# Performance work log

Hardware: AMD Instinct MI355X
Metric: run time of the kernel (lower is better)

The kernel has to match this reference:

```python
import jax, jax.numpy as jnp
import numpy as np

N_ATOMS = 524288
D = 256
B = 16384  # number of molecules (segments)
M_STEPS = 6


def setup_inputs() -> dict:
    key = jax.random.key(0)
    k1, k2, k3 = jax.random.split(key, 3)
    atom_features = jax.random.normal(k1, (N_ATOMS, D), dtype=jnp.float32)
    atom_split = jnp.sort(jax.random.randint(k2, (N_ATOMS,), 0, B, dtype=jnp.int32))
    # LSTM weights: U is (2d, 4d); bias has forget gate initialized to 1
    U = jax.random.normal(k3, (2 * D, 4 * D), dtype=jnp.float32) * (1.0 / np.sqrt(2 * D))
    b = jnp.concatenate([
        jnp.zeros((D,), jnp.float32),
        jnp.ones((D,), jnp.float32),
        jnp.zeros((D,), jnp.float32),
        jnp.zeros((D,), jnp.float32),
    ])
    return {"atom_features": atom_features, "atom_split": atom_split, "U": U, "b": b}


def _lstm_step(q_star, c, U, b):
    z = q_star @ U + b  # [B, 4d]
    i = jax.nn.sigmoid(z[:, :D])
    f = jax.nn.sigmoid(z[:, D:2 * D])
    o = jax.nn.sigmoid(z[:, 2 * D:3 * D])
    g = jnp.tanh(z[:, 3 * D:])
    c_out = f * c + i * g
    h_out = o * jnp.tanh(c_out)
    return h_out, c_out


def reference(atom_features, atom_split, U, b):
    c = jnp.zeros((B, D), jnp.float32)
    h = jnp.zeros((B, D), jnp.float32)
    q_star = None
    for _ in range(M_STEPS):
        q_expanded = h[atom_split]                     # [N, d] gather
        e = jnp.sum(atom_features * q_expanded, axis=1)  # [N]
        e_exp = jnp.exp(e)
        e_mol = jax.ops.segment_sum(e_exp, atom_split, num_segments=B)  # [B]
        a = e_exp / e_mol[atom_split]                  # segment softmax [N]
        r = jax.ops.segment_sum(a[:, None] * atom_features, atom_split, num_segments=B)  # [B, d]
        q_star = jnp.concatenate([h, r], axis=1)       # [B, 2d]
        h, c = _lstm_step(q_star, c, U, b)
    return q_star
```

## Files before the change

### kernel.cpp

```cpp
#include <hip/hip_runtime.h>
#include <hip/hip_bf16.h>
#include <math.h>

#define N_ATOMS 524288
#define DIM 256
#define NB 16384
#define M_STEPS 6

typedef _Float16 f16x8 __attribute__((ext_vector_type(8)));
typedef float f32x16 __attribute__((ext_vector_type(16)));

__device__ __forceinline__ float sigmoidf_(float z) {
    return 1.0f / (1.0f + __expf(-z));
}
__device__ __forceinline__ float tanh_fast(float z) {
    return 1.0f - 2.0f / (__expf(2.0f * z) + 1.0f);
}
__device__ __forceinline__ float2 h2f2(unsigned u) {
    union { unsigned u; _Float16 h[2]; } x; x.u = u;
    float2 r; r.x = (float)x.h[0]; r.y = (float)x.h[1]; return r;
}

__global__ void bounds_kernel(const int* __restrict__ split, int* __restrict__ lb) {
    int b = blockIdx.x * blockDim.x + threadIdx.x;
    if (b > NB) return;
    int lo = 0, hi = N_ATOMS;
    while (lo < hi) {
        int mid = (lo + hi) >> 1;
        if (split[mid] < b) lo = mid + 1; else hi = mid;
    }
    lb[b] = lo;
}

__global__ __launch_bounds__(256) void uswz_kernel(const float* __restrict__ U,
                                                   _Float16* __restrict__ uh) {
    int d = blockIdx.x * 256 + threadIdx.x;
    int f = d >> 8;
    int r = d & 255;
    int jjp = r >> 6;
    int lane = r & 63;
    int nt = f >> 5, kc = f & 31;
    int n = nt * 32 + (lane & 31);
    int k = kc * 16 + (lane >> 5) * 8 + jjp * 2;
    union { unsigned u; _Float16 h[2]; } p;
    p.h[0] = (_Float16)U[(size_t)k * 1024 + n];
    p.h[1] = (_Float16)U[(size_t)(k + 1) * 1024 + n];
    *(unsigned*)(&uh[(size_t)(f * 64 + lane) * 8 + jjp * 2]) = p.u;
}

__global__ __launch_bounds__(256) void attn0_cvt_kernel(
    const float* __restrict__ x,
    const int* __restrict__ lb,
    float* __restrict__ rout,
    _Float16* __restrict__ xh)
{
    const int t    = threadIdx.x;
    const int wave = t >> 6;
    const int lane = t & 63;
    const int b    = blockIdx.x * 4 + wave;
    const int g    = lane >> 4;
    const int q    = lane & 15;

    const int s = lb[b];
    const int e = lb[b + 1];

    float a0x=0.f,a0y=0.f,a0z=0.f,a0w=0.f;
    float a1x=0.f,a1y=0.f,a1z=0.f,a1w=0.f;
    float a2x=0.f,a2y=0.f,a2z=0.f,a2w=0.f;
    float a3x=0.f,a3y=0.f,a3z=0.f,a3w=0.f;
    float cnt = 0.f;

    for (int i = s + g; i < e; i += 4) {
        const float* xr = &x[(size_t)i * DIM + q * 16];
        const float4 c0 = *(const float4*)(xr + 0);
        const float4 c1 = *(const float4*)(xr + 4);
        const float4 c2 = *(const float4*)(xr + 8);
        const float4 c3 = *(const float4*)(xr + 12);
        cnt += 1.f;
        a0x += c0.x; a0y += c0.y; a0z += c0.z; a0w += c0.w;
        a1x += c1.x; a1y += c1.y; a1z += c1.z; a1w += c1.w;
        a2x += c2.x; a2y += c2.y; a2z += c2.z; a2w += c2.w;
        a3x += c3.x; a3y += c3.y; a3z += c3.z; a3w += c3.w;
        union { _Float16 h[16]; uint4 v[2]; } P;
        P.h[0]=(_Float16)c0.x; P.h[1]=(_Float16)c0.y; P.h[2]=(_Float16)c0.z; P.h[3]=(_Float16)c0.w;
        P.h[4]=(_Float16)c1.x; P.h[5]=(_Float16)c1.y; P.h[6]=(_Float16)c1.z; P.h[7]=(_Float16)c1.w;
        P.h[8]=(_Float16)c2.x; P.h[9]=(_Float16)c2.y; P.h[10]=(_Float16)c2.z; P.h[11]=(_Float16)c2.w;
        P.h[12]=(_Float16)c3.x; P.h[13]=(_Float16)c3.y; P.h[14]=(_Float16)c3.z; P.h[15]=(_Float16)c3.w;
        uint4* xw = (uint4*)(&xh[(size_t)i * DIM + q * 16]);
        xw[0] = P.v[0];
        xw[1] = P.v[1];
    }

#define XRED(v) { v += __shfl_xor(v, 16, 64); v += __shfl_xor(v, 32, 64); }
    XRED(a0x) XRED(a0y) XRED(a0z) XRED(a0w)
    XRED(a1x) XRED(a1y) XRED(a1z) XRED(a1w)
    XRED(a2x) XRED(a2y) XRED(a2z) XRED(a2w)
    XRED(a3x) XRED(a3y) XRED(a3z) XRED(a3w)
    XRED(cnt)
#undef XRED

    const float inv = (cnt > 0.f) ? (1.0f / cnt) : 0.f;
    float vx = (g==0) ? a0x : (g==1) ? a1x : (g==2) ? a2x : a3x;
    float vy = (g==0) ? a0y : (g==1) ? a1y : (g==2) ? a2y : a3y;
    float vz = (g==0) ? a0z : (g==1) ? a1z : (g==2) ? a2z : a3z;
    float vw = (g==0) ? a0w : (g==1) ? a1w : (g==2) ? a2w : a3w;
    float4 v; v.x = vx*inv; v.y = vy*inv; v.z = vz*inv; v.w = vw*inv;
    *(float4*)(&rout[(size_t)b * DIM + q * 16 + g * 4]) = v;
}

__global__ __launch_bounds__(256) void attn_f16_kernel(
    const _Float16* __restrict__ xhp,
    const int* __restrict__ lb,
    const float* __restrict__ h,
    float* __restrict__ rout,
    int rstride)
{
    const int t    = threadIdx.x;
    const int wave = t >> 6;
    const int lane = t & 63;
    const int b    = blockIdx.x * 4 + wave;
    const int g    = lane >> 4;
    const int q    = lane & 15;

    const int s = lb[b];
    const int e = lb[b + 1];

    const float* hrow = &h[(size_t)b * DIM + q * 16];
    const float4 hv0 = *(const float4*)(hrow + 0);
    const float4 hv1 = *(const float4*)(hrow + 4);
    const float4 hv2 = *(const float4*)(hrow + 8);
    const float4 hv3 = *(const float4*)(hrow + 12);

    float a0x=0.f,a0y=0.f,a0z=0.f,a0w=0.f;
    float a1x=0.f,a1y=0.f,a1z=0.f,a1w=0.f;
    float a2x=0.f,a2y=0.f,a2z=0.f,a2w=0.f;
    float a3x=0.f,a3y=0.f,a3z=0.f,a3w=0.f;
    float ssum = 0.f;

    int i = s + g;
    uint4 A = {0,0,0,0}, B = {0,0,0,0};
    if (i < e) {
        const uint4* xr = (const uint4*)(&xhp[(size_t)i * DIM + q * 16]);
        A = xr[0]; B = xr[1];
    }
    while (i < e) {
        const int inext = i + 4;
        const int iload = (inext < e) ? inext : i;
        const uint4* xr = (const uint4*)(&xhp[(size_t)iload * DIM + q * 16]);
        const uint4 nA = xr[0];
        const uint4 nB = xr[1];

        const float2 p0 = h2f2(A.x), p1 = h2f2(A.y), p2 = h2f2(A.z), p3 = h2f2(A.w);
        const float2 p4 = h2f2(B.x), p5 = h2f2(B.y), p6 = h2f2(B.z), p7 = h2f2(B.w);
        const float4 c0 = {p0.x, p0.y, p1.x, p1.y};
        const float4 c1 = {p2.x, p2.y, p3.x, p3.y};
        const float4 c2 = {p4.x, p4.y, p5.x, p5.y};
        const float4 c3 = {p6.x, p6.y, p7.x, p7.y};

        float d01 = c0.x*hv0.x + c0.y*hv0.y + c0.z*hv0.z + c0.w*hv0.w
                  + c1.x*hv1.x + c1.y*hv1.y + c1.z*hv1.z + c1.w*hv1.w;
        float d23 = c2.x*hv2.x + c2.y*hv2.y + c2.z*hv2.z + c2.w*hv2.w
                  + c3.x*hv3.x + c3.y*hv3.y + c3.z*hv3.z + c3.w*hv3.w;
        float d = d01 + d23;
        d += __shfl_xor(d, 1, 64);
        d += __shfl_xor(d, 2, 64);
        d += __shfl_xor(d, 4, 64);
        d += __shfl_xor(d, 8, 64);
        const float ee = __expf(d);
        ssum += ee;
        a0x += ee*c0.x; a0y += ee*c0.y; a0z += ee*c0.z; a0w += ee*c0.w;
        a1x += ee*c1.x; a1y += ee*c1.y; a1z += ee*c1.z; a1w += ee*c1.w;
        a2x += ee*c2.x; a2y += ee*c2.y; a2z += ee*c2.z; a2w += ee*c2.w;
        a3x += ee*c3.x; a3y += ee*c3.y; a3z += ee*c3.z; a3w += ee*c3.w;

        A = nA; B = nB;
        i = inext;
    }

#define XRED(v) { v += __shfl_xor(v, 16, 64); v += __shfl_xor(v, 32, 64); }
    XRED(a0x) XRED(a0y) XRED(a0z) XRED(a0w)
    XRED(a1x) XRED(a1y) XRED(a1z) XRED(a1w)
    XRED(a2x) XRED(a2y) XRED(a2z) XRED(a2w)
    XRED(a3x) XRED(a3y) XRED(a3z) XRED(a3w)
    XRED(ssum)
#undef XRED

    const float inv = (ssum > 0.f) ? (1.0f / ssum) : 0.f;
    float vx = (g==0) ? a0x : (g==1) ? a1x : (g==2) ? a2x : a3x;
    float vy = (g==0) ? a0y : (g==1) ? a1y : (g==2) ? a2y : a3y;
    float vz = (g==0) ? a0z : (g==1) ? a1z : (g==2) ? a2z : a3z;
    float vw = (g==0) ? a0w : (g==1) ? a1w : (g==2) ? a2w : a3w;
    float4 v; v.x = vx*inv; v.y = vy*inv; v.z = vz*inv; v.w = vw*inv;
    *(float4*)(&rout[(size_t)b * rstride + q * 16 + g * 4]) = v;
}

#define LBM 128
#define LBK 64
#define APAD 8
__global__ __launch_bounds__(256, 2) void lstm_mfma_kernel(
    const float* __restrict__ h_in,
    const float* __restrict__ r,
    const _Float16* __restrict__ uh,
    const float* __restrict__ bias,
    float* __restrict__ c,
    float* __restrict__ h_out,
    float* __restrict__ hdup,
    int kb0)
{
    __shared__ _Float16 As[LBM][LBK + APAD];
    __shared__ _Float16 Bs[8 * 4 * 512];

    const int t = threadIdx.x;
    const int w = t >> 6;
    const int lane = t & 63;
    const int m0 = blockIdx.y * LBM;
    const int bx = blockIdx.x;

    f32x16 acc[8];
    #pragma unroll
    for (int et = 0; et < 8; ++et)
        #pragma unroll
        for (int q = 0; q < 16; ++q) acc[et][q] = 0.0f;

    for (int kb = kb0; kb < 8; ++kb) {
        const float* A = (kb < 4) ? h_in : r;
        const int ak = (kb & 3) * LBK;
        __syncthreads();
        #pragma unroll
        for (int i = 0; i < 8; ++i) {
            int idx = i * 256 + t;
            int row = idx >> 4, k4 = idx & 15;
            float4 v = *(const float4*)(&A[(size_t)(m0 + row) * DIM + ak + k4 * 4]);
            union { _Float16 h[4]; ushort4 u; } bh;
            bh.h[0] = (_Float16)v.x; bh.h[1] = (_Float16)v.y;
            bh.h[2] = (_Float16)v.z; bh.h[3] = (_Float16)v.w;
            *(ushort4*)(&As[row][k4 * 4]) = bh.u;
        }
        #pragma unroll
        for (int run = 0; run < 8; ++run) {
            const int nt = (run >> 1) * 8 + bx * 2 + (run & 1);
            const uint4 v = ((const uint4*)(uh + (size_t)(nt * 32 + kb * 4) * 512))[t];
            *(uint4*)(&Bs[run * 2048 + t * 8]) = v;
        }
        __syncthreads();
        #pragma unroll
        for (int kc = 0; kc < 4; ++kc) {
            f16x8 af = *(const f16x8*)(&As[w * 32 + (lane & 31)][kc * 16 + (lane >> 5) * 8]);
            #pragma unroll
            for (int et = 0; et < 8; ++et) {
                f16x8 bh = *(const f16x8*)(&Bs[et * 2048 + kc * 512 + lane * 8]);
                acc[et] = __builtin_amdgcn_mfma_f32_32x32x16_f16(af, bh, acc[et], 0, 0, 0);
            }
        }
    }

    const int col32 = lane & 31;
    const int rbase = m0 + w * 32 + 4 * (lane >> 5);
    #pragma unroll
    for (int jh = 0; jh < 2; ++jh) {
        const int col = bx * 64 + jh * 32 + col32;
        const float bi = bias[col];
        const float bf_ = bias[256 + col];
        const float bo = bias[512 + col];
        const float bg = bias[768 + col];
        const f32x16 zi = acc[0 * 2 + jh];
        const f32x16 zf = acc[1 * 2 + jh];
        const f32x16 zo = acc[2 * 2 + jh];
        const f32x16 zg = acc[3 * 2 + jh];
        #pragma unroll
        for (int reg = 0; reg < 16; ++reg) {
            const int row = rbase + (reg & 3) + 8 * (reg >> 2);
            const size_t idx = (size_t)row * DIM + col;
            const float ig = sigmoidf_(zi[reg] + bi);
            const float fg = sigmoidf_(zf[reg] + bf_);
            const float og = sigmoidf_(zo[reg] + bo);
            const float gg = tanh_fast(zg[reg] + bg);
            const float cn = fg * c[idx] + ig * gg;
            c[idx] = cn;
            const float hn = og * tanh_fast(cn);
            h_out[idx] = hn;
            if (hdup) hdup[(size_t)row * 512 + col] = hn;
        }
    }
}

extern "C" void kernel_launch(void* const* d_in, const int* in_sizes, int n_in,
                              void* d_out, int out_size, void* d_ws, size_t ws_size,
                              hipStream_t stream) {
    const float* x     = (const float*)d_in[0];
    const int*   split = (const int*)d_in[1];
    const float* U     = (const float*)d_in[2];
    const float* bias  = (const float*)d_in[3];
    float* out = (float*)d_out;

    char* ws = (char*)d_ws;
    const size_t lb_bytes  = ((size_t)(NB + 1) * sizeof(int) + 255) & ~(size_t)255;
    const size_t mat_bytes = (size_t)NB * DIM * sizeof(float);
    int*   lb   = (int*)ws;
    float* hA   = (float*)(ws + lb_bytes);
    float* hB   = (float*)(ws + lb_bytes + mat_bytes);
    float* cbuf = (float*)(ws + lb_bytes + 2 * mat_bytes);
    float* rbuf = (float*)(ws + lb_bytes + 3 * mat_bytes);
    _Float16* uh = (_Float16*)(ws + lb_bytes + 4 * mat_bytes);
    _Float16* xh = (_Float16*)(ws + lb_bytes + 4 * mat_bytes + (1 << 20));

    bounds_kernel<<<(NB + 1 + 255) / 256, 256, 0, stream>>>(split, lb);
    uswz_kernel<<<1024, 256, 0, stream>>>(U, uh);
    hipMemsetAsync(cbuf, 0, mat_bytes, stream);

    float* h_cur = hA;
    float* h_nxt = hB;
    for (int m = 0; m < M_STEPS; ++m) {
        const bool last = (m == M_STEPS - 1);
        float* rdst   = last ? (out + DIM) : rbuf;
        int    rstrid = last ? (2 * DIM) : DIM;
        if (m == 0) {
            attn0_cvt_kernel<<<NB / 4, 256, 0, stream>>>(x, lb, rbuf, xh);
        } else {
            attn_f16_kernel<<<NB / 4, 256, 0, stream>>>(xh, lb, h_cur, rdst, rstrid);
        }
        if (!last) {
            dim3 grid(4, NB / LBM);
            float* hdup = (m == M_STEPS - 2) ? out : (float*)nullptr;
            lstm_mfma_kernel<<<grid, 256, 0, stream>>>(
                (m == 0) ? rbuf : h_cur, rbuf, uh, bias, cbuf, h_nxt, hdup,
                (m == 0) ? 4 : 0);
            float* tmp = h_cur; h_cur = h_nxt; h_nxt = tmp;
        }
    }
}
```

Baseline: 1.275 ms.

## Fuse all Set2Set steps into one persistent kernel with on-chip LSTM state

Replaces the per-step attention and LSTM kernel launches with a single kernel in which each 512-thread block owns 64 molecules for all steps. The h, r and c state stays in LDS (h and r as fp16), so the global round trips for h, c and r and the launch gaps between steps go away, and the c memset is dropped. The trade-offs: each block now streams the whole U matrix from global or L2 on every step instead of staging it in LDS, the grid shrinks to 256 blocks at one block per CU, and keeping h in fp16 may cost some accuracy.

```diff
diff --git a/kernel.cpp b/kernel.cpp
--- a/kernel.cpp
+++ b/kernel.cpp
@@ -6,6 +6,11 @@
 #define DIM 256
 #define NB 16384
 #define M_STEPS 6
+
+#define SEG 64
+#define NTHREADS 512
+#define SEGW 8
+#define AST 520
 
 typedef _Float16 f16x8 __attribute__((ext_vector_type(8)));
 typedef float f32x16 __attribute__((ext_vector_type(16)));
@@ -48,240 +53,225 @@
     *(unsigned*)(&uh[(size_t)(f * 64 + lane) * 8 + jjp * 2]) = p.u;
 }
 
-__global__ __launch_bounds__(256) void attn0_cvt_kernel(
+__global__ __launch_bounds__(NTHREADS, 1) void set2set_fused_kernel(
     const float* __restrict__ x,
     const int* __restrict__ lb,
-    float* __restrict__ rout,
-    _Float16* __restrict__ xh)
+    const _Float16* __restrict__ uh,
+    const float* __restrict__ bias,
+    _Float16* __restrict__ xh,
+    float* __restrict__ out)
 {
+    extern __shared__ char smem[];
+    _Float16 (*A)[AST]  = (_Float16(*)[AST])smem;
+    float    (*Cs)[DIM] = (float(*)[DIM])(smem + SEG * AST * 2);
+    int*     lbs        = (int*)(smem + SEG * AST * 2 + SEG * DIM * 4);
+
     const int t    = threadIdx.x;
-    const int wave = t >> 6;
+    const int w    = t >> 6;
     const int lane = t & 63;
-    const int b    = blockIdx.x * 4 + wave;
     const int g    = lane >> 4;
     const int q    = lane & 15;
-
-    const int s = lb[b];
-    const int e = lb[b + 1];
-
-    float a0x=0.f,a0y=0.f,a0z=0.f,a0w=0.f;
-    float a1x=0.f,a1y=0.f,a1z=0.f,a1w=0.f;
-    float a2x=0.f,a2y=0.f,a2z=0.f,a2w=0.f;
-    float a3x=0.f,a3y=0.f,a3z=0.f,a3w=0.f;
-    float cnt = 0.f;
-
-    for (int i = s + g; i < e; i += 4) {
-        const float* xr = &x[(size_t)i * DIM + q * 16];
-        const float4 c0 = *(const float4*)(xr + 0);
-        const float4 c1 = *(const float4*)(xr + 4);
-        const float4 c2 = *(const float4*)(xr + 8);
-        const float4 c3 = *(const float4*)(xr + 12);
-        cnt += 1.f;
-        a0x += c0.x; a0y += c0.y; a0z += c0.z; a0w += c0.w;
-        a1x += c1.x; a1y += c1.y; a1z += c1.z; a1w += c1.w;
-        a2x += c2.x; a2y += c2.y; a2z += c2.z; a2w += c2.w;
-        a3x += c3.x; a3y += c3.y; a3z += c3.z; a3w += c3.w;
-        union { _Float16 h[16]; uint4 v[2]; } P;
-        P.h[0]=(_Float16)c0.x; P.h[1]=(_Float16)c0.y; P.h[2]=(_Float16)c0.z; P.h[3]=(_Float16)c0.w;
-        P.h[4]=(_Float16)c1.x; P.h[5]=(_Float16)c1.y; P.h[6]=(_Float16)c1.z; P.h[7]=(_Float16)c1.w;
-        P.h[8]=(_Float16)c2.x; P.h[9]=(_Float16)c2.y; P.h[10]=(_Float16)c2.z; P.h[11]=(_Float16)c2.w;
-        P.h[12]=(_Float16)c3.x; P.h[13]=(_Float16)c3.y; P.h[14]=(_Float16)c3.z; P.h[15]=(_Float16)c3.w;
-        uint4* xw = (uint4*)(&xh[(size_t)i * DIM + q * 16]);
-        xw[0] = P.v[0];
-        xw[1] = P.v[1];
-    }
+    const int s0seg = blockIdx.x * SEG;
+
+    if (t <= SEG) lbs[t] = lb[s0seg + t];
+    for (int idx = t; idx < SEG * 64; idx += NTHREADS) {
+        int row = idx >> 6, j4 = idx & 63;
+        uint2 z; z.x = 0u; z.y = 0u;
+        *(uint2*)(&A[row][j4 * 4]) = z;
+        float4 zf = {0.f, 0.f, 0.f, 0.f};
+        *(float4*)(&Cs[row][j4 * 4]) = zf;
+    }
+    const int col32 = lane & 31;
+    const int d     = w * 32 + col32;
+    const float bi  = bias[d];
+    const float bf_ = bias[256 + d];
+    const float bo  = bias[512 + d];
+    const float bg  = bias[768 + d];
+    __syncthreads();
 
 #define XRED(v) { v += __shfl_xor(v, 16, 64); v += __shfl_xor(v, 32, 64); }
-    XRED(a0x) XRED(a0y) XRED(a0z) XRED(a0w)
-    XRED(a1x) XRED(a1y) XRED(a1z) XRED(a1w)
-    XRED(a2x) XRED(a2y) XRED(a2z) XRED(a2w)
-    XRED(a3x) XRED(a3y) XRED(a3z) XRED(a3w)
-    XRED(cnt)
+
+    for (int js = 0; js < SEGW; ++js) {
+        const int sl = w * SEGW + js;
+        const int s = lbs[sl], e = lbs[sl + 1];
+        float a0x=0.f,a0y=0.f,a0z=0.f,a0w=0.f;
+        float a1x=0.f,a1y=0.f,a1z=0.f,a1w=0.f;
+        float a2x=0.f,a2y=0.f,a2z=0.f,a2w=0.f;
+        float a3x=0.f,a3y=0.f,a3z=0.f,a3w=0.f;
+        float cnt = 0.f;
+        int i = s + g;
+        float4 c0={0,0,0,0}, c1={0,0,0,0}, c2={0,0,0,0}, c3={0,0,0,0};
+        if (i < e) {
+            const float* xr = &x[(size_t)i * DIM + q * 16];
+            c0 = *(const float4*)(xr + 0);  c1 = *(const float4*)(xr + 4);
+            c2 = *(const float4*)(xr + 8);  c3 = *(const float4*)(xr + 12);
+        }
+        while (i < e) {
+            const int inext = i + 4;
+            const int iload = (inext < e) ? inext : i;
+            const float* xr = &x[(size_t)iload * DIM + q * 16];
+            const float4 n0 = *(const float4*)(xr + 0);
+            const float4 n1 = *(const float4*)(xr + 4);
+            const float4 n2 = *(const float4*)(xr + 8);
+            const float4 n3 = *(const float4*)(xr + 12);
+
+            union { _Float16 h[16]; uint4 v[2]; } P;
+            P.h[0]=(_Float16)c0.x; P.h[1]=(_Float16)c0.y; P.h[2]=(_Float16)c0.z; P.h[3]=(_Float16)c0.w;
+            P.h[4]=(_Float16)c1.x; P.h[5]=(_Float16)c1.y; P.h[6]=(_Float16)c1.z; P.h[7]=(_Float16)c1.w;
+            P.h[8]=(_Float16)c2.x; P.h[9]=(_Float16)c2.y; P.h[10]=(_Float16)c2.z; P.h[11]=(_Float16)c2.w;
+            P.h[12]=(_Float16)c3.x; P.h[13]=(_Float16)c3.y; P.h[14]=(_Float16)c3.z; P.h[15]=(_Float16)c3.w;
+            uint4* xw = (uint4*)(&xh[(size_t)i * DIM + q * 16]);
+            xw[0] = P.v[0]; xw[1] = P.v[1];
+
+            cnt += 1.f;
+            a0x += c0.x; a0y += c0.y; a0z += c0.z; a0w += c0.w;
+            a1x += c1.x; a1y += c1.y; a1z += c1.z; a1w += c1.w;
+            a2x += c2.x; a2y += c2.y; a2z += c2.z; a2w += c2.w;
+            a3x += c3.x; a3y += c3.y; a3z += c3.z; a3w += c3.w;
+            c0=n0; c1=n1; c2=n2; c3=n3;
+            i = inext;
+        }
+        XRED(a0x) XRED(a0y) XRED(a0z) XRED(a0w)
+        XRED(a1x) XRED(a1y) XRED(a1z) XRED(a1w)
+        XRED(a2x) XRED(a2y) XRED(a2z) XRED(a2w)
+        XRED(a3x) XRED(a3y) XRED(a3z) XRED(a3w)
+        XRED(cnt)
+        const float inv = (cnt > 0.f) ? (1.0f / cnt) : 0.f;
+        float vx = (g==0) ? a0x : (g==1) ? a1x : (g==2) ? a2x : a3x;
+        float vy = (g==0) ? a0y : (g==1) ? a1y : (g==2) ? a2y : a3y;
+        float vz = (g==0) ? a0z : (g==1) ? a1z : (g==2) ? a2z : a3z;
+        float vw = (g==0) ? a0w : (g==1) ? a1w : (g==2) ? a2w : a3w;
+        union { _Float16 h[4]; uint2 u; } R;
+        R.h[0]=(_Float16)(vx*inv); R.h[1]=(_Float16)(vy*inv);
+        R.h[2]=(_Float16)(vz*inv); R.h[3]=(_Float16)(vw*inv);
+        *(uint2*)(&A[sl][256 + q * 16 + g * 4]) = R.u;
+    }
+    __syncthreads();
+
+    for (int m = 0; m < M_STEPS - 1; ++m) {
+        f32x16 acc[8];
+        #pragma unroll
+        for (int et = 0; et < 8; ++et)
+            #pragma unroll
+            for (int qq = 0; qq < 16; ++qq) acc[et][qq] = 0.0f;
+
+        #pragma unroll 4
+        for (int kc = 0; kc < 32; ++kc) {
+            const int kof = kc * 16 + (lane >> 5) * 8;
+            f16x8 af0 = *(const f16x8*)(&A[(lane & 31)][kof]);
+            f16x8 af1 = *(const f16x8*)(&A[32 + (lane & 31)][kof]);
+            #pragma unroll
+            for (int gate = 0; gate < 4; ++gate) {
+                const int nt = gate * 8 + w;
+                f16x8 bfr = *(const f16x8*)(&uh[(size_t)(nt * 32 + kc) * 512 + lane * 8]);
+                acc[gate * 2 + 0] = __builtin_amdgcn_mfma_f32_32x32x16_f16(af0, bfr, acc[gate * 2 + 0], 0, 0, 0);
+                acc[gate * 2 + 1] = __builtin_amdgcn_mfma_f32_32x32x16_f16(af1, bfr, acc[gate * 2 + 1], 0, 0, 0);
+            }
+        }
+        __syncthreads();
+
+        #pragma unroll
+        for (int mt = 0; mt < 2; ++mt) {
+            const int rb = mt * 32 + 4 * (lane >> 5);
+            #pragma unroll
+            for (int reg = 0; reg < 16; ++reg) {
+                const int row = rb + (reg & 3) + 8 * (reg >> 2);
+                const float ig = sigmoidf_(acc[0 + mt][reg] + bi);
+                const float fg = sigmoidf_(acc[2 + mt][reg] + bf_);
+                const float og = sigmoidf_(acc[4 + mt][reg] + bo);
+                const float gg = tanh_fast(acc[6 + mt][reg] + bg);
+                const float cn = fg * Cs[row][d] + ig * gg;
+                Cs[row][d] = cn;
+                const float hn = og * tanh_fast(cn);
+                A[row][d] = (_Float16)hn;
+                if (m == M_STEPS - 2)
+                    out[(size_t)(s0seg + row) * 512 + d] = hn;
+            }
+        }
+        __syncthreads();
+
+        const bool last = (m == M_STEPS - 2);
+        for (int js = 0; js < SEGW; ++js) {
+            const int sl = w * SEGW + js;
+            const int s = lbs[sl], e = lbs[sl + 1];
+
+            const uint4* hr = (const uint4*)(&A[sl][q * 16]);
+            const uint4 H0 = hr[0], H1 = hr[1];
+            const float2 h0 = h2f2(H0.x), h1 = h2f2(H0.y), h2_ = h2f2(H0.z), h3 = h2f2(H0.w);
+            const float2 h4 = h2f2(H1.x), h5 = h2f2(H1.y), h6 = h2f2(H1.z), h7 = h2f2(H1.w);
+            const float4 hv0 = {h0.x, h0.y, h1.x, h1.y};
+            const float4 hv1 = {h2_.x, h2_.y, h3.x, h3.y};
+            const float4 hv2 = {h4.x, h4.y, h5.x, h5.y};
+            const float4 hv3 = {h6.x, h6.y, h7.x, h7.y};
+
+            float a0x=0.f,a0y=0.f,a0z=0.f,a0w=0.f;
+            float a1x=0.f,a1y=0.f,a1z=0.f,a1w=0.f;
+            float a2x=0.f,a2y=0.f,a2z=0.f,a2w=0.f;
+            float a3x=0.f,a3y=0.f,a3z=0.f,a3w=0.f;
+            float ssum = 0.f;
+
+            int i = s + g;
+            uint4 Au = {0,0,0,0}, Bu = {0,0,0,0};
+            if (i < e) {
+                const uint4* xr = (const uint4*)(&xh[(size_t)i * DIM + q * 16]);
+                Au = xr[0]; Bu = xr[1];
+            }
+            while (i < e) {
+                const int inext = i + 4;
+                const int iload = (inext < e) ? inext : i;
+                const uint4* xr = (const uint4*)(&xh[(size_t)iload * DIM + q * 16]);
+                const uint4 nA = xr[0];
+                const uint4 nB = xr[1];
+
+                const float2 p0 = h2f2(Au.x), p1 = h2f2(Au.y), p2 = h2f2(Au.z), p3 = h2f2(Au.w);
+                const float2 p4 = h2f2(Bu.x), p5 = h2f2(Bu.y), p6 = h2f2(Bu.z), p7 = h2f2(Bu.w);
+                const float4 c0 = {p0.x, p0.y, p1.x, p1.y};
+                const float4 c1 = {p2.x, p2.y, p3.x, p3.y};
+                const float4 c2 = {p4.x, p4.y, p5.x, p5.y};
+                const float4 c3 = {p6.x, p6.y, p7.x, p7.y};
+
+                float d01 = c0.x*hv0.x + c0.y*hv0.y + c0.z*hv0.z + c0.w*hv0.w
+                          + c1.x*hv1.x + c1.y*hv1.y + c1.z*hv1.z + c1.w*hv1.w;
+                float d23 = c2.x*hv2.x + c2.y*hv2.y + c2.z*hv2.z + c2.w*hv2.w
+                          + c3.x*hv3.x + c3.y*hv3.y + c3.z*hv3.z + c3.w*hv3.w;
+                float dd = d01 + d23;
+                dd += __shfl_xor(dd, 1, 64);
+                dd += __shfl_xor(dd, 2, 64);
+                dd += __shfl_xor(dd, 4, 64);
+                dd += __shfl_xor(dd, 8, 64);
+                const float ee = __expf(dd);
+                ssum += ee;
+                a0x += ee*c0.x; a0y += ee*c0.y; a0z += ee*c0.z; a0w += ee*c0.w;
+                a1x += ee*c1.x; a1y += ee*c1.y; a1z += ee*c1.z; a1w += ee*c1.w;
+                a2x += ee*c2.x; a2y += ee*c2.y; a2z += ee*c2.z; a2w += ee*c2.w;
+                a3x += ee*c3.x; a3y += ee*c3.y; a3z += ee*c3.z; a3w += ee*c3.w;
+
+                Au = nA; Bu = nB;
+                i = inext;
+            }
+            XRED(a0x) XRED(a0y) XRED(a0z) XRED(a0w)
+            XRED(a1x) XRED(a1y) XRED(a1z) XRED(a1w)
+            XRED(a2x) XRED(a2y) XRED(a2z) XRED(a2w)
+            XRED(a3x) XRED(a3y) XRED(a3z) XRED(a3w)
+            XRED(ssum)
+            const float inv = (ssum > 0.f) ? (1.0f / ssum) : 0.f;
+            float vx = (g==0) ? a0x : (g==1) ? a1x : (g==2) ? a2x : a3x;
+            float vy = (g==0) ? a0y : (g==1) ? a1y : (g==2) ? a2y : a3y;
+            float vz = (g==0) ? a0z : (g==1) ? a1z : (g==2) ? a2z : a3z;
+            float vw = (g==0) ? a0w : (g==1) ? a1w : (g==2) ? a2w : a3w;
+            if (last) {
+                float4 v; v.x = vx*inv; v.y = vy*inv; v.z = vz*inv; v.w = vw*inv;
+                *(float4*)(&out[(size_t)(s0seg + sl) * 512 + 256 + q * 16 + g * 4]) = v;
+            } else {
+                union { _Float16 h[4]; uint2 u; } R;
+                R.h[0]=(_Float16)(vx*inv); R.h[1]=(_Float16)(vy*inv);
+                R.h[2]=(_Float16)(vz*inv); R.h[3]=(_Float16)(vw*inv);
+                *(uint2*)(&A[sl][256 + q * 16 + g * 4]) = R.u;
+            }
+        }
+        if (m < M_STEPS - 2) __syncthreads();
+    }
 #undef XRED
-
-    const float inv = (cnt > 0.f) ? (1.0f / cnt) : 0.f;
-    float vx = (g==0) ? a0x : (g==1) ? a1x : (g==2) ? a2x : a3x;
-    float vy = (g==0) ? a0y : (g==1) ? a1y : (g==2) ? a2y : a3y;
-    float vz = (g==0) ? a0z : (g==1) ? a1z : (g==2) ? a2z : a3z;
-    float vw = (g==0) ? a0w : (g==1) ? a1w : (g==2) ? a2w : a3w;
-    float4 v; v.x = vx*inv; v.y = vy*inv; v.z = vz*inv; v.w = vw*inv;
-    *(float4*)(&rout[(size_t)b * DIM + q * 16 + g * 4]) = v;
-}
-
-__global__ __launch_bounds__(256) void attn_f16_kernel(
-    const _Float16* __restrict__ xhp,
-    const int* __restrict__ lb,
-    const float* __restrict__ h,
-    float* __restrict__ rout,
-    int rstride)
-{
-    const int t    = threadIdx.x;
-    const int wave = t >> 6;
-    const int lane = t & 63;
-    const int b    = blockIdx.x * 4 + wave;
-    const int g    = lane >> 4;
-    const int q    = lane & 15;
-
-    const int s = lb[b];
-    const int e = lb[b + 1];
-
-    const float* hrow = &h[(size_t)b * DIM + q * 16];
-    const float4 hv0 = *(const float4*)(hrow + 0);
-    const float4 hv1 = *(const float4*)(hrow + 4);
-    const float4 hv2 = *(const float4*)(hrow + 8);
-    const float4 hv3 = *(const float4*)(hrow + 12);
-
-    float a0x=0.f,a0y=0.f,a0z=0.f,a0w=0.f;
-    float a1x=0.f,a1y=0.f,a1z=0.f,a1w=0.f;
-    float a2x=0.f,a2y=0.f,a2z=0.f,a2w=0.f;
-    float a3x=0.f,a3y=0.f,a3z=0.f,a3w=0.f;
-    float ssum = 0.f;
-
-    int i = s + g;
-    uint4 A = {0,0,0,0}, B = {0,0,0,0};
-    if (i < e) {
-        const uint4* xr = (const uint4*)(&xhp[(size_t)i * DIM + q * 16]);
-        A = xr[0]; B = xr[1];
-    }
-    while (i < e) {
-        const int inext = i + 4;
-        const int iload = (inext < e) ? inext : i;
-        const uint4* xr = (const uint4*)(&xhp[(size_t)iload * DIM + q * 16]);
-        const uint4 nA = xr[0];
-        const uint4 nB = xr[1];
-
-        const float2 p0 = h2f2(A.x), p1 = h2f2(A.y), p2 = h2f2(A.z), p3 = h2f2(A.w);
-        const float2 p4 = h2f2(B.x), p5 = h2f2(B.y), p6 = h2f2(B.z), p7 = h2f2(B.w);
-        const float4 c0 = {p0.x, p0.y, p1.x, p1.y};
-        const float4 c1 = {p2.x, p2.y, p3.x, p3.y};
-        const float4 c2 = {p4.x, p4.y, p5.x, p5.y};
-        const float4 c3 = {p6.x, p6.y, p7.x, p7.y};
-
-        float d01 = c0.x*hv0.x + c0.y*hv0.y + c0.z*hv0.z + c0.w*hv0.w
-                  + c1.x*hv1.x + c1.y*hv1.y + c1.z*hv1.z + c1.w*hv1.w;
-        float d23 = c2.x*hv2.x + c2.y*hv2.y + c2.z*hv2.z + c2.w*hv2.w
-                  + c3.x*hv3.x + c3.y*hv3.y + c3.z*hv3.z + c3.w*hv3.w;
-        float d = d01 + d23;
-        d += __shfl_xor(d, 1, 64);
-        d += __shfl_xor(d, 2, 64);
-        d += __shfl_xor(d, 4, 64);
-        d += __shfl_xor(d, 8, 64);
-        const float ee = __expf(d);
-        ssum += ee;
-        a0x += ee*c0.x; a0y += ee*c0.y; a0z += ee*c0.z; a0w += ee*c0.w;
-        a1x += ee*c1.x; a1y += ee*c1.y; a1z += ee*c1.z; a1w += ee*c1.w;
-        a2x += ee*c2.x; a2y += ee*c2.y; a2z += ee*c2.z; a2w += ee*c2.w;
-        a3x += ee*c3.x; a3y += ee*c3.y; a3z += ee*c3.z; a3w += ee*c3.w;
-
-        A = nA; B = nB;
-        i = inext;
-    }
-
-#define XRED(v) { v += __shfl_xor(v, 16, 64); v += __shfl_xor(v, 32, 64); }
-    XRED(a0x) XRED(a0y) XRED(a0z) XRED(a0w)
-    XRED(a1x) XRED(a1y) XRED(a1z) XRED(a1w)
-    XRED(a2x) XRED(a2y) XRED(a2z) XRED(a2w)
-    XRED(a3x) XRED(a3y) XRED(a3z) XRED(a3w)
-    XRED(ssum)
-#undef XRED
-
-    const float inv = (ssum > 0.f) ? (1.0f / ssum) : 0.f;
-    float vx = (g==0) ? a0x : (g==1) ? a1x : (g==2) ? a2x : a3x;
-    float vy = (g==0) ? a0y : (g==1) ? a1y : (g==2) ? a2y : a3y;
-    float vz = (g==0) ? a0z : (g==1) ? a1z : (g==2) ? a2z : a3z;
-    float vw = (g==0) ? a0w : (g==1) ? a1w : (g==2) ? a2w : a3w;
-    float4 v; v.x = vx*inv; v.y = vy*inv; v.z = vz*inv; v.w = vw*inv;
-    *(float4*)(&rout[(size_t)b * rstride + q * 16 + g * 4]) = v;
-}
-
-#define LBM 128
-#define LBK 64
-#define APAD 8
-__global__ __launch_bounds__(256, 2) void lstm_mfma_kernel(
-    const float* __restrict__ h_in,
-    const float* __restrict__ r,
-    const _Float16* __restrict__ uh,
-    const float* __restrict__ bias,
-    float* __restrict__ c,
-    float* __restrict__ h_out,
-    float* __restrict__ hdup,
-    int kb0)
-{
-    __shared__ _Float16 As[LBM][LBK + APAD];
-    __shared__ _Float16 Bs[8 * 4 * 512];
-
-    const int t = threadIdx.x;
-    const int w = t >> 6;
-    const int lane = t & 63;
-    const int m0 = blockIdx.y * LBM;
-    const int bx = blockIdx.x;
-
-    f32x16 acc[8];
-    #pragma unroll
-    for (int et = 0; et < 8; ++et)
-        #pragma unroll
-        for (int q = 0; q < 16; ++q) acc[et][q] = 0.0f;
-
-    for (int kb = kb0; kb < 8; ++kb) {
-        const float* A = (kb < 4) ? h_in : r;
-        const int ak = (kb & 3) * LBK;
-        __syncthreads();
-        #pragma unroll
-        for (int i = 0; i < 8; ++i) {
-            int idx = i * 256 + t;
-            int row = idx >> 4, k4 = idx & 15;
-            float4 v = *(const float4*)(&A[(size_t)(m0 + row) * DIM + ak + k4 * 4]);
-            union { _Float16 h[4]; ushort4 u; } bh;
-            bh.h[0] = (_Float16)v.x; bh.h[1] = (_Float16)v.y;
-            bh.h[2] = (_Float16)v.z; bh.h[3] = (_Float16)v.w;
-            *(ushort4*)(&As[row][k4 * 4]) = bh.u;
-        }
-        #pragma unroll
-        for (int run = 0; run < 8; ++run) {
-            const int nt = (run >> 1) * 8 + bx * 2 + (run & 1);
-            const uint4 v = ((const uint4*)(uh + (size_t)(nt * 32 + kb * 4) * 512))[t];
-            *(uint4*)(&Bs[run * 2048 + t * 8]) = v;
-        }
-        __syncthreads();
-        #pragma unroll
-        for (int kc = 0; kc < 4; ++kc) {
-            f16x8 af = *(const f16x8*)(&As[w * 32 + (lane & 31)][kc * 16 + (lane >> 5) * 8]);
-            #pragma unroll
-            for (int et = 0; et < 8; ++et) {
-                f16x8 bh = *(const f16x8*)(&Bs[et * 2048 + kc * 512 + lane * 8]);
-                acc[et] = __builtin_amdgcn_mfma_f32_32x32x16_f16(af, bh, acc[et], 0, 0, 0);
-            }
-        }
-    }
-
-    const int col32 = lane & 31;
-    const int rbase = m0 + w * 32 + 4 * (lane >> 5);
-    #pragma unroll
-    for (int jh = 0; jh < 2; ++jh) {
-        const int col = bx * 64 + jh * 32 + col32;
-        const float bi = bias[col];
-        const float bf_ = bias[256 + col];
-        const float bo = bias[512 + col];
-        const float bg = bias[768 + col];
-        const f32x16 zi = acc[0 * 2 + jh];
-        const f32x16 zf = acc[1 * 2 + jh];
-        const f32x16 zo = acc[2 * 2 + jh];
-        const f32x16 zg = acc[3 * 2 + jh];
-        #pragma unroll
-        for (int reg = 0; reg < 16; ++reg) {
-            const int row = rbase + (reg & 3) + 8 * (reg >> 2);
-            const size_t idx = (size_t)row * DIM + col;
-            const float ig = sigmoidf_(zi[reg] + bi);
-            const float fg = sigmoidf_(zf[reg] + bf_);
-            const float og = sigmoidf_(zo[reg] + bo);
-            const float gg = tanh_fast(zg[reg] + bg);
-            const float cn = fg * c[idx] + ig * gg;
-            c[idx] = cn;
-            const float hn = og * tanh_fast(cn);
-            h_out[idx] = hn;
-            if (hdup) hdup[(size_t)row * 512 + col] = hn;
-        }
-    }
 }
 
 extern "C" void kernel_launch(void* const* d_in, const int* in_sizes, int n_in,
@@ -294,38 +284,15 @@
     float* out = (float*)d_out;
 
     char* ws = (char*)d_ws;
-    const size_t lb_bytes  = ((size_t)(NB + 1) * sizeof(int) + 255) & ~(size_t)255;
-    const size_t mat_bytes = (size_t)NB * DIM * sizeof(float);
-    int*   lb   = (int*)ws;
-    float* hA   = (float*)(ws + lb_bytes);
-    float* hB   = (float*)(ws + lb_bytes + mat_bytes);
-    float* cbuf = (float*)(ws + lb_bytes + 2 * mat_bytes);
-    float* rbuf = (float*)(ws + lb_bytes + 3 * mat_bytes);
-    _Float16* uh = (_Float16*)(ws + lb_bytes + 4 * mat_bytes);
-    _Float16* xh = (_Float16*)(ws + lb_bytes + 4 * mat_bytes + (1 << 20));
+    const size_t lb_bytes = ((size_t)(NB + 1) * sizeof(int) + 255) & ~(size_t)255;
+    int*      lb = (int*)ws;
+    _Float16* uh = (_Float16*)(ws + lb_bytes);
+    _Float16* xh = (_Float16*)(ws + lb_bytes + (1 << 20));
 
     bounds_kernel<<<(NB + 1 + 255) / 256, 256, 0, stream>>>(split, lb);
     uswz_kernel<<<1024, 256, 0, stream>>>(U, uh);
-    hipMemsetAsync(cbuf, 0, mat_bytes, stream);
-
-    float* h_cur = hA;
-    float* h_nxt = hB;
-    for (int m = 0; m < M_STEPS; ++m) {
-        const bool last = (m == M_STEPS - 1);
-        float* rdst   = last ? (out + DIM) : rbuf;
-        int    rstrid = last ? (2 * DIM) : DIM;
-        if (m == 0) {
-            attn0_cvt_kernel<<<NB / 4, 256, 0, stream>>>(x, lb, rbuf, xh);
-        } else {
-            attn_f16_kernel<<<NB / 4, 256, 0, stream>>>(xh, lb, h_cur, rdst, rstrid);
-        }
-        if (!last) {
-            dim3 grid(4, NB / LBM);
-            float* hdup = (m == M_STEPS - 2) ? out : (float*)nullptr;
-            lstm_mfma_kernel<<<grid, 256, 0, stream>>>(
-                (m == 0) ? rbuf : h_cur, rbuf, uh, bias, cbuf, h_nxt, hdup,
-                (m == 0) ? 4 : 0);
-            float* tmp = h_cur; h_cur = h_nxt; h_nxt = tmp;
-        }
-    }
-}
+
+    const int smem_bytes = SEG * AST * 2 + SEG * DIM * 4 + (SEG + 1) * 4;
+    set2set_fused_kernel<<<NB / SEG, NTHREADS, smem_bytes, stream>>>(
+        x, lb, uh, bias, xh, out);
+}
```

After: 1.244 ms. -2.5%, faster.
